# Kernel tuning notes

Hardware: AMD Instinct MI355X
Metric: run time of the kernel (lower is better)

## Reference

```python
import jax, jax.numpy as jnp
import numpy as np

# DenseKAN defaults from tfkan
GRID_SIZE = 5
SPLINE_ORDER = 3
GRID_MIN, GRID_MAX = -1.0, 1.0
KH = KW = 3  # kernel_size


def _grid():
    h = (GRID_MAX - GRID_MIN) / GRID_SIZE
    # grid_size + 2*spline_order + 1 knots, extended beyond grid_range
    return jnp.linspace(GRID_MIN - SPLINE_ORDER * h, GRID_MAX + SPLINE_ORDER * h,
                        GRID_SIZE + 2 * SPLINE_ORDER + 1, dtype=jnp.float32)


def _spline_basis(x, grid, order):
    # x: (N, in_size) -> (N, in_size, grid_size + spline_order) via Cox-de Boor
    x = x[..., None]
    b = ((x >= grid[:-1]) & (x < grid[1:])).astype(x.dtype)
    for k in range(1, order + 1):
        b = ((x - grid[:-(k + 1)]) / (grid[k:-1] - grid[:-(k + 1)]) * b[..., :-1]
             + (grid[k + 1:] - x) / (grid[k + 1:] - grid[1:-k]) * b[..., 1:])
    return b


def _extract_patches(x):
    # VALID, stride 1; TF extract_patches flattens feature dim as [kh, kw, C]
    B, H, W, C = x.shape
    Ho, Wo = H - KH + 1, W - KW + 1
    p = jnp.stack([x[:, di:di + Ho, dj:dj + Wo, :]
                   for di in range(KH) for dj in range(KW)], axis=3)  # (B,Ho,Wo,KH*KW,C)
    return p.reshape(B, Ho, Wo, KH * KW * C)


def setup_inputs() -> dict:
    key = jax.random.key(0)
    k = jax.random.split(key, 5)
    B, H, W, C = 32, 32, 32, 32
    F = 128
    in_size = KH * KW * C
    basis = GRID_SIZE + SPLINE_ORDER
    return {
        "x": jax.random.normal(k[0], (B, H, W, C), jnp.float32),
        "spline_kernel": jax.random.normal(k[1], (in_size, basis, F), jnp.float32) * 0.1,
        "scale_factor": jax.random.normal(k[2], (in_size, F), jnp.float32) * 0.1,
        "kan_bias": jnp.zeros((F,), jnp.float32),
        "conv_bias": jnp.zeros((F,), jnp.float32),
    }


def reference(x, spline_kernel, scale_factor, kan_bias, conv_bias):
    grid = _grid()
    pat = _extract_patches(x)                 # (B, Ho, Wo, in_size)
    B, Ho, Wo, In = pat.shape
    xf = pat.reshape(-1, In)                  # (N, in_size)
    sb = _spline_basis(xf, grid, SPLINE_ORDER)  # (N, in_size, basis)
    # phi(x) = scale * (spline(x) + silu(x)); output = sum_i phi_i + biases
    # fused: never materialize the (N, in_size, units) tensor
    w = spline_kernel * scale_factor[:, None, :]        # (in_size, basis, units)
    out = (jnp.einsum('nik,iko->no', sb, w)
           + jax.nn.silu(xf) @ scale_factor
           + kan_bias)                                   # (N, units)
    out = out.reshape(B, Ho, Wo, -1) + conv_bias
    return out
```

## Files before the change

### kernel.cpp

```cpp
#include <hip/hip_runtime.h>
#include <hip/hip_bf16.h>


#define C_IN   32
#define F_OUT  128
#define BATCH  32
#define HIN    32
#define WIN    32
#define HO_    30
#define WO_    30
#define NPIX   (BATCH*HO_*WO_)
#define NELEM  (BATCH*HIN*WIN*C_IN)
#define NBASIS 9
#define KCHUNKS 81
#define FEAT_BYTES  ((size_t)NELEM*NBASIS*2)
#define WPACK_BYTES ((size_t)KCHUNKS*F_OUT*32*2)

typedef __attribute__((ext_vector_type(8))) short short8;
typedef __attribute__((ext_vector_type(4))) float f32x4;

#define GLOAD_LDS16(g, l) \
  __builtin_amdgcn_global_load_lds((const __attribute__((address_space(1))) void*)(g), \
                                   (__attribute__((address_space(3))) void*)(l), 16, 0, 0)

__global__ __launch_bounds__(256) void kan_featurize(
    const float* __restrict__ x, __hip_bfloat16* __restrict__ feat) {
  int idx = blockIdx.x * 256 + threadIdx.x;
  float v = x[idx];

  float b0[11], b1[10], b2[9], b3[8];
#pragma unroll
  for (int j = 0; j < 11; ++j) {
    float gj  = -2.2f + 0.4f * (float)j;
    float gj1 = -2.2f + 0.4f * (float)(j + 1);
    b0[j] = (v >= gj && v < gj1) ? 1.0f : 0.0f;
  }
#pragma unroll
  for (int j = 0; j < 10; ++j) {
    float gj = -2.2f + 0.4f * (float)j;
    b1[j] = (v - gj) * 2.5f * b0[j] + ((gj + 0.8f) - v) * 2.5f * b0[j + 1];
  }
#pragma unroll
  for (int j = 0; j < 9; ++j) {
    float gj = -2.2f + 0.4f * (float)j;
    b2[j] = (v - gj) * 1.25f * b1[j] + ((gj + 1.2f) - v) * 1.25f * b1[j + 1];
  }
#pragma unroll
  for (int j = 0; j < 8; ++j) {
    float gj = -2.2f + 0.4f * (float)j;
    b3[j] = (v - gj) * (1.0f/1.2f) * b2[j] + ((gj + 1.6f) - v) * (1.0f/1.2f) * b2[j + 1];
  }
  float sil = v / (1.0f + __expf(-v));

  int bhw = idx >> 5, c = idx & 31;
  __hip_bfloat16* o = feat + (size_t)bhw * (NBASIS * 32) + c;
#pragma unroll
  for (int k = 0; k < 8; ++k) o[k * 32] = __float2bfloat16(b3[k]);
  o[8 * 32] = __float2bfloat16(sil);
}

__global__ __launch_bounds__(256) void kan_pack_w(
    const float* __restrict__ sk, const float* __restrict__ sf,
    __hip_bfloat16* __restrict__ wp) {
  int tid = blockIdx.x * 256 + threadIdx.x;
  int csub = tid & 31;
  int col  = (tid >> 5) & 127;
  int kc   = tid >> 12;
  int dd = kc / 9, k = kc - dd * 9;
  int i = dd * 32 + csub;
  float w = sf[i * 128 + col];
  if (k < 8) w *= sk[(i * 8 + k) * 128 + col];
  int part = csub >> 3, within = csub & 7;
  int slot = part ^ ((col >> 1) & 3);
  wp[(size_t)kc * 4096 + col * 32 + slot * 8 + within] = __float2bfloat16(w);
}

__global__ __launch_bounds__(256) void kan_gemm(
    const __hip_bfloat16* __restrict__ featb, const __hip_bfloat16* __restrict__ wpb,
    const float* __restrict__ kbias, const float* __restrict__ cbias,
    float* __restrict__ out) {
  __shared__ char lds[49152];
  const char* feat = (const char*)featb;
  const char* wp   = (const char*)wpb;

  int tid  = threadIdx.x;
  int lane = tid & 63, wid = tid >> 6;
  int wm = wid >> 1, wn = wid & 1;
  int q = lane >> 4, fr = lane & 15;

  int orig = blockIdx.x;
  int xcd = orig & 7, sub = orig >> 3;
  int swz = (xcd < 2 ? xcd * 57 : 114 + (xcd - 2) * 56) + sub;
  int mb = swz * 64;

  int arow = tid >> 2, aslot = tid & 3;
  int apix = mb + arow;
  int wo = apix % 30, t30 = apix / 30;
  int ho = t30 % 30,  bb  = t30 / 30;
  const char* asrc = feat + (size_t)((bb * 32 + ho) * 32 + wo) * 576
                          + (size_t)((aslot ^ ((arow >> 1) & 3)) * 16);

  int ar0 = 32 * wm + fr, ar1 = ar0 + 16;
  int aoff0 = ar0 * 64 + ((q ^ ((ar0 >> 1) & 3)) * 16);
  int aoff1 = ar1 * 64 + ((q ^ ((ar1 >> 1) & 3)) * 16);
  int boff[4];
#pragma unroll
  for (int n = 0; n < 4; ++n) {
    int col = 64 * wn + 16 * n + fr;
    boff[n] = col * 64 + ((q ^ ((col >> 1) & 3)) * 16);
  }

  f32x4 acc[2][4];
#pragma unroll
  for (int m = 0; m < 2; ++m)
#pragma unroll
    for (int n = 0; n < 4; ++n) acc[m][n] = (f32x4)(0.0f);

  auto stage = [&](int kc) {
    int s = kc & 3;
    int dd = kc / 9, k = kc - dd * 9;
    int di = dd / 3, dj = dd - di * 3;
    int au = (di * 32 + dj) * 576 + k * 64;
    GLOAD_LDS16(asrc + au, lds + s * 4096 + tid * 16);
    const char* wsrc = wp + (size_t)kc * 8192 + tid * 16;
    GLOAD_LDS16(wsrc,        lds + 16384 + s * 8192 + tid * 16);
    GLOAD_LDS16(wsrc + 4096, lds + 16384 + s * 8192 + 4096 + tid * 16);
  };

  auto compute = [&](int s) {
    const char* A = lds + s * 4096;
    const char* B = lds + 16384 + s * 8192;
    short8 a0 = *(const short8*)(A + aoff0);
    short8 a1 = *(const short8*)(A + aoff1);
#pragma unroll
    for (int n = 0; n < 4; ++n) {
      short8 bn = *(const short8*)(B + boff[n]);
      acc[0][n] = __builtin_amdgcn_mfma_f32_16x16x32_bf16(a0, bn, acc[0][n], 0, 0, 0);
      acc[1][n] = __builtin_amdgcn_mfma_f32_16x16x32_bf16(a1, bn, acc[1][n], 0, 0, 0);
    }
  };

  stage(0); stage(1); stage(2);
  asm volatile("s_waitcnt vmcnt(6)" ::: "memory");
  __builtin_amdgcn_s_barrier();
  __builtin_amdgcn_sched_barrier(0);

  for (int kc = 0; kc < KCHUNKS - 3; ++kc) {
    stage(kc + 3);
    compute(kc & 3);
    asm volatile("s_waitcnt vmcnt(6) lgkmcnt(0)" ::: "memory");
    __builtin_amdgcn_s_barrier();
    __builtin_amdgcn_sched_barrier(0);
  }
  asm volatile("s_waitcnt vmcnt(0)" ::: "memory");
  __builtin_amdgcn_s_barrier();
  __builtin_amdgcn_sched_barrier(0);
  compute((KCHUNKS - 3) & 3);
  compute((KCHUNKS - 2) & 3);
  compute((KCHUNKS - 1) & 3);

#pragma unroll
  for (int n = 0; n < 4; ++n) {
    int col = 64 * wn + 16 * n + fr;
    float bias = kbias[col] + cbias[col];
#pragma unroll
    for (int m = 0; m < 2; ++m) {
      int row = mb + 32 * wm + 16 * m + q * 4;
      f32x4 v = acc[m][n];
#pragma unroll
      for (int r = 0; r < 4; ++r)
        out[(size_t)(row + r) * 128 + col] = v[r] + bias;
    }
  }
}

extern "C" void kernel_launch(void* const* d_in, const int* in_sizes, int n_in,
                              void* d_out, int out_size, void* d_ws, size_t ws_size,
                              hipStream_t stream) {
  const float* x  = (const float*)d_in[0];
  const float* sk = (const float*)d_in[1];
  const float* sf = (const float*)d_in[2];
  const float* kb = (const float*)d_in[3];
  const float* cb = (const float*)d_in[4];
  float* out = (float*)d_out;

  char* ws = (char*)d_ws;
  __hip_bfloat16* feat = (__hip_bfloat16*)ws;
  __hip_bfloat16* wpk  = (__hip_bfloat16*)(ws + FEAT_BYTES);

  hipLaunchKernelGGL(kan_featurize, dim3(NELEM / 256), dim3(256), 0, stream, x, feat);
  hipLaunchKernelGGL(kan_pack_w, dim3((KCHUNKS * F_OUT * 32) / 256), dim3(256), 0, stream,
                     sk, sf, wpk);
  hipLaunchKernelGGL(kan_gemm, dim3(NPIX / 64), dim3(256), 0, stream,
                     feat, wpk, kb, cb, out);
}
```

Before: 112.1 us.

## Vectorize featurize and weight-pack stores, deepen GEMM pipeline to six stages

The featurize kernel now has each thread handle 8 channels, reading them with vector loads and writing 16-byte packed bf16 rows per basis instead of scattered 2-byte stores. The weight pack kernel likewise builds a short8 per thread and writes it with one 16-byte store. The GEMM's LDS ring grows from 4 to 6 stages, with 5 chunks in flight and setprio raised around the MFMA block, to hide more global load latency. The bigger LDS footprint (72KB) may lower the number of blocks resident per CU.

```diff
diff --git a/kernel.cpp b/kernel.cpp
--- a/kernel.cpp
+++ b/kernel.cpp
@@ -19,16 +19,16 @@
 typedef __attribute__((ext_vector_type(8))) short short8;
 typedef __attribute__((ext_vector_type(4))) float f32x4;
 
+__device__ __forceinline__ short bf16_bits(float v) {
+  return __builtin_bit_cast(short, __float2bfloat16(v));
+}
+
 #define GLOAD_LDS16(g, l) \
   __builtin_amdgcn_global_load_lds((const __attribute__((address_space(1))) void*)(g), \
                                    (__attribute__((address_space(3))) void*)(l), 16, 0, 0)
 
-__global__ __launch_bounds__(256) void kan_featurize(
-    const float* __restrict__ x, __hip_bfloat16* __restrict__ feat) {
-  int idx = blockIdx.x * 256 + threadIdx.x;
-  float v = x[idx];
-
-  float b0[11], b1[10], b2[9], b3[8];
+__device__ __forceinline__ void kan_basis(float v, float* o9) {
+  float b0[11], b1[10], b2[9];
 #pragma unroll
   for (int j = 0; j < 11; ++j) {
     float gj  = -2.2f + 0.4f * (float)j;
@@ -48,38 +48,59 @@
 #pragma unroll
   for (int j = 0; j < 8; ++j) {
     float gj = -2.2f + 0.4f * (float)j;
-    b3[j] = (v - gj) * (1.0f/1.2f) * b2[j] + ((gj + 1.6f) - v) * (1.0f/1.2f) * b2[j + 1];
-  }
-  float sil = v / (1.0f + __expf(-v));
-
-  int bhw = idx >> 5, c = idx & 31;
-  __hip_bfloat16* o = feat + (size_t)bhw * (NBASIS * 32) + c;
-#pragma unroll
-  for (int k = 0; k < 8; ++k) o[k * 32] = __float2bfloat16(b3[k]);
-  o[8 * 32] = __float2bfloat16(sil);
+    o9[j] = (v - gj) * (1.0f/1.2f) * b2[j] + ((gj + 1.6f) - v) * (1.0f/1.2f) * b2[j + 1];
+  }
+  o9[8] = v / (1.0f + __expf(-v));
+}
+
+__global__ __launch_bounds__(256) void kan_featurize(
+    const float* __restrict__ x, __hip_bfloat16* __restrict__ feat) {
+  int t = blockIdx.x * 256 + threadIdx.x;
+  int bhw = t >> 2, c0 = (t & 3) * 8;
+  const f32x4* xp = (const f32x4*)(x + ((size_t)bhw * 32 + c0));
+  f32x4 v0 = xp[0], v1 = xp[1];
+  float f[8][9];
+#pragma unroll
+  for (int j = 0; j < 4; ++j) kan_basis(v0[j], f[j]);
+#pragma unroll
+  for (int j = 0; j < 4; ++j) kan_basis(v1[j], f[4 + j]);
+
+  char* o = (char*)feat + (size_t)bhw * 576 + c0 * 2;
+#pragma unroll
+  for (int k = 0; k < 9; ++k) {
+    short8 s;
+#pragma unroll
+    for (int j = 0; j < 8; ++j)
+      s[j] = bf16_bits(f[j][k]);
+    *(short8*)(o + k * 64) = s;
+  }
 }
 
 __global__ __launch_bounds__(256) void kan_pack_w(
     const float* __restrict__ sk, const float* __restrict__ sf,
     __hip_bfloat16* __restrict__ wp) {
-  int tid = blockIdx.x * 256 + threadIdx.x;
-  int csub = tid & 31;
-  int col  = (tid >> 5) & 127;
-  int kc   = tid >> 12;
+  int t = blockIdx.x * 256 + threadIdx.x;
+  int part = t & 3;
+  int col  = (t >> 2) & 127;
+  int kc   = t >> 9;
   int dd = kc / 9, k = kc - dd * 9;
-  int i = dd * 32 + csub;
-  float w = sf[i * 128 + col];
-  if (k < 8) w *= sk[(i * 8 + k) * 128 + col];
-  int part = csub >> 3, within = csub & 7;
+  short8 s;
+#pragma unroll
+  for (int j = 0; j < 8; ++j) {
+    int i = dd * 32 + part * 8 + j;
+    float w = sf[i * 128 + col];
+    if (k < 8) w *= sk[(i * 8 + k) * 128 + col];
+    s[j] = bf16_bits(w);
+  }
   int slot = part ^ ((col >> 1) & 3);
-  wp[(size_t)kc * 4096 + col * 32 + slot * 8 + within] = __float2bfloat16(w);
+  *(short8*)((char*)wp + (size_t)kc * 8192 + col * 64 + slot * 16) = s;
 }
 
 __global__ __launch_bounds__(256) void kan_gemm(
     const __hip_bfloat16* __restrict__ featb, const __hip_bfloat16* __restrict__ wpb,
     const float* __restrict__ kbias, const float* __restrict__ cbias,
     float* __restrict__ out) {
-  __shared__ char lds[49152];
+  __shared__ char lds[73728];
   const char* feat = (const char*)featb;
   const char* wp   = (const char*)wpb;
 
@@ -117,47 +138,51 @@
     for (int n = 0; n < 4; ++n) acc[m][n] = (f32x4)(0.0f);
 
   auto stage = [&](int kc) {
-    int s = kc & 3;
+    int s = kc % 6;
     int dd = kc / 9, k = kc - dd * 9;
     int di = dd / 3, dj = dd - di * 3;
     int au = (di * 32 + dj) * 576 + k * 64;
     GLOAD_LDS16(asrc + au, lds + s * 4096 + tid * 16);
     const char* wsrc = wp + (size_t)kc * 8192 + tid * 16;
-    GLOAD_LDS16(wsrc,        lds + 16384 + s * 8192 + tid * 16);
-    GLOAD_LDS16(wsrc + 4096, lds + 16384 + s * 8192 + 4096 + tid * 16);
+    GLOAD_LDS16(wsrc,        lds + 24576 + s * 8192 + tid * 16);
+    GLOAD_LDS16(wsrc + 4096, lds + 24576 + s * 8192 + 4096 + tid * 16);
   };
 
   auto compute = [&](int s) {
     const char* A = lds + s * 4096;
-    const char* B = lds + 16384 + s * 8192;
+    const char* B = lds + 24576 + s * 8192;
     short8 a0 = *(const short8*)(A + aoff0);
     short8 a1 = *(const short8*)(A + aoff1);
+    __builtin_amdgcn_s_setprio(1);
 #pragma unroll
     for (int n = 0; n < 4; ++n) {
       short8 bn = *(const short8*)(B + boff[n]);
       acc[0][n] = __builtin_amdgcn_mfma_f32_16x16x32_bf16(a0, bn, acc[0][n], 0, 0, 0);
       acc[1][n] = __builtin_amdgcn_mfma_f32_16x16x32_bf16(a1, bn, acc[1][n], 0, 0, 0);
     }
+    __builtin_amdgcn_s_setprio(0);
   };
 
-  stage(0); stage(1); stage(2);
-  asm volatile("s_waitcnt vmcnt(6)" ::: "memory");
+  stage(0); stage(1); stage(2); stage(3); stage(4);
+  asm volatile("s_waitcnt vmcnt(12)" ::: "memory");
   __builtin_amdgcn_s_barrier();
   __builtin_amdgcn_sched_barrier(0);
 
-  for (int kc = 0; kc < KCHUNKS - 3; ++kc) {
-    stage(kc + 3);
-    compute(kc & 3);
-    asm volatile("s_waitcnt vmcnt(6) lgkmcnt(0)" ::: "memory");
+  for (int kc = 0; kc < KCHUNKS - 5; ++kc) {
+    stage(kc + 5);
+    compute(kc % 6);
+    asm volatile("s_waitcnt vmcnt(12) lgkmcnt(0)" ::: "memory");
     __builtin_amdgcn_s_barrier();
     __builtin_amdgcn_sched_barrier(0);
   }
   asm volatile("s_waitcnt vmcnt(0)" ::: "memory");
   __builtin_amdgcn_s_barrier();
   __builtin_amdgcn_sched_barrier(0);
-  compute((KCHUNKS - 3) & 3);
-  compute((KCHUNKS - 2) & 3);
-  compute((KCHUNKS - 1) & 3);
+  compute((KCHUNKS - 5) % 6);
+  compute((KCHUNKS - 4) % 6);
+  compute((KCHUNKS - 3) % 6);
+  compute((KCHUNKS - 2) % 6);
+  compute((KCHUNKS - 1) % 6);
 
 #pragma unroll
   for (int n = 0; n < 4; ++n) {
@@ -188,8 +213,8 @@
   __hip_bfloat16* feat = (__hip_bfloat16*)ws;
   __hip_bfloat16* wpk  = (__hip_bfloat16*)(ws + FEAT_BYTES);
 
-  hipLaunchKernelGGL(kan_featurize, dim3(NELEM / 256), dim3(256), 0, stream, x, feat);
-  hipLaunchKernelGGL(kan_pack_w, dim3((KCHUNKS * F_OUT * 32) / 256), dim3(256), 0, stream,
+  hipLaunchKernelGGL(kan_featurize, dim3(NELEM / 8 / 256), dim3(256), 0, stream, x, feat);
+  hipLaunchKernelGGL(kan_pack_w, dim3((KCHUNKS * F_OUT * 32 / 8) / 256), dim3(256), 0, stream,
                      sk, sf, wpk);
   hipLaunchKernelGGL(kan_gemm, dim3(NPIX / 64), dim3(256), 0, stream,
                      feat, wpk, kb, cb, out);
```

Measured after the change: 114.6 us. 1.02x slower.
